# Optimization experiments

Hardware: AMD Instinct MI355X
Metric: run time of the kernel (lower is better)

The kernel has to match this reference:

```python
import jax, jax.numpy as jnp
import numpy as np

N_NODES = 50000
N_EDGES = 600000
D_IN, D_HID, D_OUT = 128, 256, 128


def setup_inputs() -> dict:
    key = jax.random.key(0)
    ks = jax.random.split(key, 8)
    x = jax.random.normal(ks[0], (N_NODES, D_IN), dtype=jnp.float32)
    edge_index = jax.random.randint(ks[1], (2, N_EDGES), 0, N_NODES, dtype=jnp.int64)
    # init_method='uniform' -> edge_weights initialized to ones
    edge_weights = jnp.ones((N_EDGES,), dtype=jnp.float32)
    def lin(k, din, dout):
        s = 1.0 / np.sqrt(din)
        return jax.random.uniform(k, (din, dout), jnp.float32, -s, s)
    W1 = lin(ks[2], D_IN, D_HID)
    b1 = jnp.zeros((D_HID,), jnp.float32)
    W2 = lin(ks[3], D_HID, D_HID)
    b2 = jnp.zeros((D_HID,), jnp.float32)
    W3 = lin(ks[4], D_HID, D_OUT)
    b3 = jnp.zeros((D_OUT,), jnp.float32)
    return {"x": x, "edge_index": edge_index, "edge_weights": edge_weights,
            "W1": W1, "b1": b1, "W2": W2, "b2": b2, "W3": W3, "b3": b3}


def reference(x, edge_index, edge_weights, W1, b1, W2, b2, W3, b3):
    N = x.shape[0]
    # learnable metric: softplus on raw edge weights
    ew = jax.nn.softplus(edge_weights)
    src, dst = edge_index[0], edge_index[1]
    # GCNConv default: add self-loops with weight 1.0
    loop = jnp.arange(N, dtype=edge_index.dtype)
    s = jnp.concatenate([src, loop])
    d = jnp.concatenate([dst, loop])
    w = jnp.concatenate([ew, jnp.ones((N,), ew.dtype)])
    # symmetric degree normalization (gcn_norm); identical edge_weight across layers
    deg = jax.ops.segment_sum(w, d, num_segments=N)
    dinv = jnp.where(deg > 0, jax.lax.rsqrt(deg), jnp.zeros_like(deg))
    norm = dinv[s] * w * dinv[d]  # [E+N]

    def gcn_conv(h, W, b):
        h = h @ W                              # [N, dout]
        msg = h[s] * norm[:, None]             # gather + scale: [E+N, dout]
        out = jax.ops.segment_sum(msg, d, num_segments=N)  # scatter-add
        return out + b

    h = jax.nn.relu(gcn_conv(x, W1, b1))   # dropout p=0.0 -> identity
    h = jax.nn.relu(gcn_conv(h, W2, b2))
    return gcn_conv(h, W3, b3)
```

## Files before the change

### kernel.cpp

```cpp
#include <hip/hip_runtime.h>
#include <hip/hip_fp16.h>
#include <math.h>

#define N_NODES 50000
#define N_EDGES 600000
#define D_IN    128
#define D_HID   256
#define D_OUT   128
#define NB_SCAN ((N_NODES + 255) / 256)

typedef unsigned short u16;
typedef __attribute__((ext_vector_type(8))) _Float16 f16x8;
typedef __attribute__((ext_vector_type(4))) float f32x4;

__device__ __forceinline__ u16 f2h(float x) {
    __half h = __float2half_rn(x);
    return *reinterpret_cast<u16*>(&h);
}
__device__ __forceinline__ float h2f(u16 h) {
    __half hh = *reinterpret_cast<__half*>(&h);
    return __half2float(hh);
}
__device__ __forceinline__ float2 h2f2(unsigned int raw) {
    __half2 h = *reinterpret_cast<__half2*>(&raw);
    return __half22float2(h);
}


__global__ void k_edge_prep(const int* __restrict__ src, const int* __restrict__ dst,
                            const float* __restrict__ w, float* __restrict__ ew,
                            float* __restrict__ deg, int* __restrict__ cnt) {
    int e = blockIdx.x * blockDim.x + threadIdx.x;
    if (e >= N_EDGES) return;
    float x = w[e];
    float sp = fmaxf(x, 0.f) + log1pf(expf(-fabsf(x)));
    ew[e] = sp;
    int d = dst[e];
    atomicAdd(&deg[d], sp);
    atomicAdd(&cnt[d], 1);
    (void)src;
}

__global__ void k_dinv(float* __restrict__ deg) {
    int n = blockIdx.x * blockDim.x + threadIdx.x;
    if (n >= N_NODES) return;
    deg[n] = rsqrtf(deg[n] + 1.0f);
}

__global__ void k_scan1(const int* __restrict__ cnt, int* __restrict__ rowptr,
                        int* __restrict__ bsum) {
    __shared__ int s[256];
    int b = blockIdx.x, t = threadIdx.x;
    int i = b * 256 + t;
    int v = (i < N_NODES) ? cnt[i] : 0;
    s[t] = v;
    __syncthreads();
    for (int off = 1; off < 256; off <<= 1) {
        int u = (t >= off) ? s[t - off] : 0;
        __syncthreads();
        s[t] += u;
        __syncthreads();
    }
    if (i < N_NODES) rowptr[i] = s[t] - v;
    if (t == 255) bsum[b] = s[255];
}

__global__ void k_scan2(const int* __restrict__ bsum, int* __restrict__ boff) {
    __shared__ int s[256];
    int t = threadIdx.x;
    int v = (t < NB_SCAN) ? bsum[t] : 0;
    s[t] = v;
    __syncthreads();
    for (int off = 1; off < 256; off <<= 1) {
        int u = (t >= off) ? s[t - off] : 0;
        __syncthreads();
        s[t] += u;
        __syncthreads();
    }
    if (t < NB_SCAN) boff[t] = s[t] - v;
    if (t == 255) boff[NB_SCAN] = s[255];
}

__global__ void k_scan3(int* __restrict__ rowptr, const int* __restrict__ boff) {
    int b = blockIdx.x, t = threadIdx.x;
    int i = b * 256 + t;
    if (i < N_NODES) rowptr[i] += boff[b];
    if (i == 0) rowptr[N_NODES] = boff[NB_SCAN];
}

__global__ void k_fill(const int* __restrict__ src, const int* __restrict__ dst,
                       const float* __restrict__ ew, const float* __restrict__ dinv,
                       const int* __restrict__ rowptr, int* __restrict__ fill,
                       int2* __restrict__ ecsr) {
    int e = blockIdx.x * blockDim.x + threadIdx.x;
    if (e >= N_EDGES) return;
    int d = dst[e];
    int s = src[e];
    int pos = rowptr[d] + atomicAdd(&fill[d], 1);
    float w = dinv[s] * ew[e] * dinv[d];
    ecsr[pos] = make_int2(s, __float_as_int(w));
}


#define WPREP_TOTAL 131072

__global__ void k_wprep(const float* __restrict__ W1, const float* __restrict__ W2,
                        const float* __restrict__ W3,
                        u16* __restrict__ B1, u16* __restrict__ B2, u16* __restrict__ B3) {
    int idx = blockIdx.x * blockDim.x + threadIdx.x;
    const float* W; u16* B; int K, N, base;
    if (idx < 32768)       { W = W1; B = B1; K = 128; N = 256; base = 0; }
    else if (idx < 98304)  { W = W2; B = B2; K = 256; N = 256; base = 32768; }
    else if (idx < 131072) { W = W3; B = B3; K = 256; N = 128; base = 98304; }
    else return;
    int p = idx - base;
    int n = p % N, k = p / N;
    float x = W[(size_t)k * N + n];
    u16 hi = f2h(x);
    u16 lo = f2h(x - h2f(hi));
    B[(size_t)n * (2 * K) + k] = hi;
    B[(size_t)n * (2 * K) + K + k] = lo;
}


template <int D, int INF, int OUTM, bool BIAS>
__global__ __launch_bounds__(256) void k_agg(const void* __restrict__ inv,
                                             const int* __restrict__ rowptr,
                                             const int2* __restrict__ ecsr,
                                             const float* __restrict__ dinv,
                                             const float* __restrict__ bias,
                                             void* __restrict__ outv) {
    int node = blockIdx.x * 4 + (threadIdx.x >> 6);
    int lane = threadIdx.x & 63;
    if (node >= N_NODES) return;
    float dn = dinv[node];
    float dd = dn * dn;
    int beg = rowptr[node], end = rowptr[node + 1];

    if (D == 256) {
        const float* inf = (const float*)inv;
        const u16* inh = (const u16*)inv;
        float sx, sy, sz, sw;
        if (INF == 0) {
            float4 sv = *(reinterpret_cast<const float4*>(inf + (size_t)node * D) + lane);
            sx = sv.x; sy = sv.y; sz = sv.z; sw = sv.w;
        } else {
            uint2 raw = *reinterpret_cast<const uint2*>(inh + (size_t)node * D + lane * 4);
            float2 f01 = h2f2(raw.x), f23 = h2f2(raw.y);
            sx = f01.x; sy = f01.y; sz = f23.x; sw = f23.y;
        }
        float ax = dd * sx, ay = dd * sy, az = dd * sz, aw = dd * sw;
        int p = beg;
        for (; p + 4 <= end; p += 4) {
            int2 e0 = ecsr[p], e1 = ecsr[p + 1], e2 = ecsr[p + 2], e3 = ecsr[p + 3];
            float w0 = __int_as_float(e0.y), w1 = __int_as_float(e1.y);
            float w2 = __int_as_float(e2.y), w3 = __int_as_float(e3.y);
            if (INF == 0) {
                float4 r0 = *(reinterpret_cast<const float4*>(inf + (size_t)e0.x * D) + lane);
                float4 r1 = *(reinterpret_cast<const float4*>(inf + (size_t)e1.x * D) + lane);
                float4 r2 = *(reinterpret_cast<const float4*>(inf + (size_t)e2.x * D) + lane);
                float4 r3 = *(reinterpret_cast<const float4*>(inf + (size_t)e3.x * D) + lane);
                ax += w0 * r0.x; ay += w0 * r0.y; az += w0 * r0.z; aw += w0 * r0.w;
                ax += w1 * r1.x; ay += w1 * r1.y; az += w1 * r1.z; aw += w1 * r1.w;
                ax += w2 * r2.x; ay += w2 * r2.y; az += w2 * r2.z; aw += w2 * r2.w;
                ax += w3 * r3.x; ay += w3 * r3.y; az += w3 * r3.z; aw += w3 * r3.w;
            } else {
                uint2 q0 = *reinterpret_cast<const uint2*>(inh + (size_t)e0.x * D + lane * 4);
                uint2 q1 = *reinterpret_cast<const uint2*>(inh + (size_t)e1.x * D + lane * 4);
                uint2 q2 = *reinterpret_cast<const uint2*>(inh + (size_t)e2.x * D + lane * 4);
                uint2 q3 = *reinterpret_cast<const uint2*>(inh + (size_t)e3.x * D + lane * 4);
                float2 a0 = h2f2(q0.x), b0 = h2f2(q0.y);
                float2 a1 = h2f2(q1.x), b1 = h2f2(q1.y);
                float2 a2 = h2f2(q2.x), b2 = h2f2(q2.y);
                float2 a3 = h2f2(q3.x), b3 = h2f2(q3.y);
                ax += w0 * a0.x; ay += w0 * a0.y; az += w0 * b0.x; aw += w0 * b0.y;
                ax += w1 * a1.x; ay += w1 * a1.y; az += w1 * b1.x; aw += w1 * b1.y;
                ax += w2 * a2.x; ay += w2 * a2.y; az += w2 * b2.x; aw += w2 * b2.y;
                ax += w3 * a3.x; ay += w3 * a3.y; az += w3 * b3.x; aw += w3 * b3.y;
            }
        }
        for (; p < end; p++) {
            int2 e0 = ecsr[p];
            float w0 = __int_as_float(e0.y);
            if (INF == 0) {
                float4 r0 = *(reinterpret_cast<const float4*>(inf + (size_t)e0.x * D) + lane);
                ax += w0 * r0.x; ay += w0 * r0.y; az += w0 * r0.z; aw += w0 * r0.w;
            } else {
                uint2 q0 = *reinterpret_cast<const uint2*>(inh + (size_t)e0.x * D + lane * 4);
                float2 a0 = h2f2(q0.x), b0 = h2f2(q0.y);
                ax += w0 * a0.x; ay += w0 * a0.y; az += w0 * b0.x; aw += w0 * b0.y;
            }
        }
        if (OUTM == 0) {
            float* out = (float*)outv;
            if (BIAS) {
                float4 b = *(reinterpret_cast<const float4*>(bias) + lane);
                ax += b.x; ay += b.y; az += b.z; aw += b.w;
            }
            float4 res; res.x = ax; res.y = ay; res.z = az; res.w = aw;
            *(reinterpret_cast<float4*>(out + (size_t)node * D) + lane) = res;
        } else {
            u16* out = (u16*)outv;
            ushort4 hv;
            hv.x = f2h(ax); hv.y = f2h(ay); hv.z = f2h(az); hv.w = f2h(aw);
            *reinterpret_cast<ushort4*>(out + (size_t)node * D + lane * 4) = hv;
        }
    } else {
        const float* inf = (const float*)inv;
        const u16* inh = (const u16*)inv;
        float sx, sy;
        if (INF == 0) {
            float2 sv = *(reinterpret_cast<const float2*>(inf + (size_t)node * D) + lane);
            sx = sv.x; sy = sv.y;
        } else {
            unsigned int raw = *reinterpret_cast<const unsigned int*>(inh + (size_t)node * D + lane * 2);
            float2 f = h2f2(raw);
            sx = f.x; sy = f.y;
        }
        float ax = dd * sx, ay = dd * sy;
        int p = beg;
        for (; p + 4 <= end; p += 4) {
            int2 e0 = ecsr[p], e1 = ecsr[p + 1], e2 = ecsr[p + 2], e3 = ecsr[p + 3];
            float w0 = __int_as_float(e0.y), w1 = __int_as_float(e1.y);
            float w2 = __int_as_float(e2.y), w3 = __int_as_float(e3.y);
            if (INF == 0) {
                float2 r0 = *(reinterpret_cast<const float2*>(inf + (size_t)e0.x * D) + lane);
                float2 r1 = *(reinterpret_cast<const float2*>(inf + (size_t)e1.x * D) + lane);
                float2 r2 = *(reinterpret_cast<const float2*>(inf + (size_t)e2.x * D) + lane);
                float2 r3 = *(reinterpret_cast<const float2*>(inf + (size_t)e3.x * D) + lane);
                ax += w0 * r0.x; ay += w0 * r0.y;
                ax += w1 * r1.x; ay += w1 * r1.y;
                ax += w2 * r2.x; ay += w2 * r2.y;
                ax += w3 * r3.x; ay += w3 * r3.y;
            } else {
                unsigned int q0 = *reinterpret_cast<const unsigned int*>(inh + (size_t)e0.x * D + lane * 2);
                unsigned int q1 = *reinterpret_cast<const unsigned int*>(inh + (size_t)e1.x * D + lane * 2);
                unsigned int q2 = *reinterpret_cast<const unsigned int*>(inh + (size_t)e2.x * D + lane * 2);
                unsigned int q3 = *reinterpret_cast<const unsigned int*>(inh + (size_t)e3.x * D + lane * 2);
                float2 f0 = h2f2(q0), f1 = h2f2(q1), f2 = h2f2(q2), f3 = h2f2(q3);
                ax += w0 * f0.x; ay += w0 * f0.y;
                ax += w1 * f1.x; ay += w1 * f1.y;
                ax += w2 * f2.x; ay += w2 * f2.y;
                ax += w3 * f3.x; ay += w3 * f3.y;
            }
        }
        for (; p < end; p++) {
            int2 e0 = ecsr[p];
            float w0 = __int_as_float(e0.y);
            if (INF == 0) {
                float2 r0 = *(reinterpret_cast<const float2*>(inf + (size_t)e0.x * D) + lane);
                ax += w0 * r0.x; ay += w0 * r0.y;
            } else {
                unsigned int q0 = *reinterpret_cast<const unsigned int*>(inh + (size_t)e0.x * D + lane * 2);
                float2 f0 = h2f2(q0);
                ax += w0 * f0.x; ay += w0 * f0.y;
            }
        }
        if (OUTM == 0) {
            float* out = (float*)outv;
            if (BIAS) {
                float2 b = *(reinterpret_cast<const float2*>(bias) + lane);
                ax += b.x; ay += b.y;
            }
            float2 res; res.x = ax; res.y = ay;
            *(reinterpret_cast<float2*>(out + (size_t)node * D) + lane) = res;
        } else {
            u16* out = (u16*)outv;
            ushort2 hv; hv.x = f2h(ax); hv.y = f2h(ay);
            *reinterpret_cast<ushort2*>(out + (size_t)node * D + lane * 2) = hv;
        }
    }
}


template <int OUT, bool BIAS, bool RELU>
__global__ __launch_bounds__(256) void k_gemm_h(const u16* __restrict__ Ap,
                                                const u16* __restrict__ Bp,
                                                const float* __restrict__ bias,
                                                void* __restrict__ Cv,
                                                int M, int K, int NN) {
    const int KP2 = 2 * K;
    __shared__ u16 As[8 * 544];
    __shared__ u16 Bs[2 * 8 * 544];
    int tid = threadIdx.x;
    int bm = blockIdx.y * 128;
    int bn = blockIdx.x * 128;
    int l = tid & 63;
    int w = tid >> 6;
    int wr = w >> 1, wc = w & 1;

    f32x4 zero = {0.f, 0.f, 0.f, 0.f};
    f32x4 acc[4][4];
    #pragma unroll
    for (int i = 0; i < 4; i++)
        #pragma unroll
        for (int j = 0; j < 4; j++) acc[i][j] = zero;

    for (int k0 = 0; k0 < K; k0 += 32) {
        #pragma unroll
        for (int q = 0; q < 2; q++) {
            int idx = tid + q * 256;
            int r = idx >> 2, o = idx & 3;
            int gr = bm + r;
            uint4 va = make_uint4(0u, 0u, 0u, 0u);
            if (gr < M)
                va = *reinterpret_cast<const uint4*>(Ap + (size_t)gr * K + k0 + o * 8);
            *reinterpret_cast<uint4*>(&As[(r >> 4) * 544 + o * 136 + (r & 15) * 8]) = va;
        }
        #pragma unroll
        for (int q = 0; q < 4; q++) {
            int idx = tid + q * 256;
            int r = idx >> 3, oct = idx & 7;
            int hf = oct >> 2, o = oct & 3;
            uint4 vb = *reinterpret_cast<const uint4*>(
                Bp + (size_t)(bn + r) * KP2 + hf * K + k0 + o * 8);
            *reinterpret_cast<uint4*>(
                &Bs[hf * 4352 + (r >> 4) * 544 + o * 136 + (r & 15) * 8]) = vb;
        }
        __syncthreads();
        int fro = (l >> 4) * 136 + (l & 15) * 8;
        f16x8 a[4], bh[4], bl[4];
        #pragma unroll
        for (int i = 0; i < 4; i++)
            a[i] = *reinterpret_cast<const f16x8*>(&As[(wr * 4 + i) * 544 + fro]);
        #pragma unroll
        for (int j = 0; j < 4; j++) {
            bh[j] = *reinterpret_cast<const f16x8*>(&Bs[(wc * 4 + j) * 544 + fro]);
            bl[j] = *reinterpret_cast<const f16x8*>(&Bs[4352 + (wc * 4 + j) * 544 + fro]);
        }
        #pragma unroll
        for (int i = 0; i < 4; i++)
            #pragma unroll
            for (int j = 0; j < 4; j++) {
                acc[i][j] = __builtin_amdgcn_mfma_f32_16x16x32_f16(a[i], bh[j], acc[i][j], 0, 0, 0);
                acc[i][j] = __builtin_amdgcn_mfma_f32_16x16x32_f16(a[i], bl[j], acc[i][j], 0, 0, 0);
            }
        __syncthreads();
    }

    int cl = l & 15;
    int rq = (l >> 4) * 4;
    float bv[4];
    #pragma unroll
    for (int j = 0; j < 4; j++) {
        int gc = bn + wc * 64 + j * 16 + cl;
        bv[j] = BIAS ? bias[gc] : 0.f;
    }
    #pragma unroll
    for (int i = 0; i < 4; i++) {
        #pragma unroll
        for (int r = 0; r < 4; r++) {
            int grow = bm + wr * 64 + i * 16 + rq + r;
            if (grow >= M) continue;
            #pragma unroll
            for (int j = 0; j < 4; j++) {
                int gc = bn + wc * 64 + j * 16 + cl;
                float v = acc[i][j][r];
                if (BIAS) v += bv[j];
                if (RELU) v = fmaxf(v, 0.f);
                if (OUT == 0) {
                    ((float*)Cv)[(size_t)grow * NN + gc] = v;
                } else {
                    ((u16*)Cv)[(size_t)grow * NN + gc] = f2h(v);
                }
            }
        }
    }
}


extern "C" void kernel_launch(void* const* d_in, const int* in_sizes, int n_in,
                              void* d_out, int out_size, void* d_ws, size_t ws_size,
                              hipStream_t stream) {
    const float* x   = (const float*)d_in[0];
    const int*   ei  = (const int*)d_in[1];
    const float* wts = (const float*)d_in[2];
    const float* W1  = (const float*)d_in[3];
    const float* b1  = (const float*)d_in[4];
    const float* W2  = (const float*)d_in[5];
    const float* b2  = (const float*)d_in[6];
    const float* W3  = (const float*)d_in[7];
    const float* b3  = (const float*)d_in[8];
    float* out = (float*)d_out;
    const int* src = ei;
    const int* dst = ei + N_EDGES;

    float* bufA   = (float*)d_ws;
    float* bufB   = bufA + (size_t)N_NODES * D_HID;
    float* ew     = bufB + (size_t)N_NODES * D_HID;
    float* deg    = ew + N_EDGES;
    int*   cnt    = (int*)(deg + N_NODES);
    int*   fill   = cnt + N_NODES;
    int*   rowptr = fill + N_NODES;
    int2*  ecsr   = (int2*)(rowptr + (N_NODES + 2));
    u16*   Wb1    = (u16*)(ecsr + N_EDGES);
    u16*   Wb2    = Wb1 + 256 * 256;
    u16*   Wb3    = Wb2 + 256 * 512;
    int*   bsum   = (int*)(Wb3 + 128 * 512);
    int*   boff   = bsum + NB_SCAN;

    hipMemsetAsync(deg, 0, sizeof(float) * N_NODES + sizeof(int) * 2 * N_NODES, stream);

    int ethreads = 256;
    int eblocks = (N_EDGES + ethreads - 1) / ethreads;
    k_edge_prep<<<eblocks, ethreads, 0, stream>>>(src, dst, wts, ew, deg, cnt);
    k_dinv<<<(N_NODES + 255) / 256, 256, 0, stream>>>(deg);
    k_scan1<<<NB_SCAN, 256, 0, stream>>>(cnt, rowptr, bsum);
    k_scan2<<<1, 256, 0, stream>>>(bsum, boff);
    k_scan3<<<NB_SCAN, 256, 0, stream>>>(rowptr, boff);
    k_fill<<<eblocks, ethreads, 0, stream>>>(src, dst, ew, deg, rowptr, fill, ecsr);
    k_wprep<<<(WPREP_TOTAL + 255) / 256, 256, 0, stream>>>(W1, W2, W3, Wb1, Wb2, Wb3);

    int aggBlocks = (N_NODES + 3) / 4;
    int gy = (N_NODES + 127) / 128;

    k_agg<128, 0, 1, false><<<aggBlocks, 256, 0, stream>>>(x, rowptr, ecsr, deg, nullptr, bufA);
    {
        dim3 g(2, gy);
        k_gemm_h<1, true, true><<<g, 256, 0, stream>>>((const u16*)bufA, Wb1, b1, bufB,
                                                       N_NODES, D_IN, D_HID);
    }
    k_agg<256, 1, 1, false><<<aggBlocks, 256, 0, stream>>>(bufB, rowptr, ecsr, deg, nullptr, bufA);
    {
        dim3 g(2, gy);
        k_gemm_h<1, true, true><<<g, 256, 0, stream>>>((const u16*)bufA, Wb2, b2, bufB,
                                                       N_NODES, D_HID, D_HID);
    }
    {
        dim3 g(1, gy);
        k_gemm_h<1, false, false><<<g, 256, 0, stream>>>((const u16*)bufB, Wb3, nullptr, bufA,
                                                         N_NODES, D_HID, D_OUT);
    }
    k_agg<128, 1, 0, true><<<aggBlocks, 256, 0, stream>>>(bufA, rowptr, ecsr, deg, b3, out);
}
```

Baseline: 384.2 us.

## Replace float degree atomics with CSR-based degree sum and atomic-free fill

Edge preprocessing now records each edge's rank from the count atomic, which lets the CSR fill run without a second atomic pass. The float atomicAdd degree accumulation is dropped. The degree is instead summed per node from the CSR rows, and normalization becomes a separate per-node pass over the CSR. This removes a set of float atomics and the fill atomics, but adds two thread-per-node kernels with serial, uncoalesced row loops and an extra rank array.

```diff
diff --git a/kernel.cpp b/kernel.cpp
--- a/kernel.cpp
+++ b/kernel.cpp
@@ -27,24 +27,14 @@
 }
 
 
-__global__ void k_edge_prep(const int* __restrict__ src, const int* __restrict__ dst,
-                            const float* __restrict__ w, float* __restrict__ ew,
-                            float* __restrict__ deg, int* __restrict__ cnt) {
+__global__ void k_hist(const int* __restrict__ dst, const float* __restrict__ w,
+                       float* __restrict__ ew, int* __restrict__ rank,
+                       int* __restrict__ cnt) {
     int e = blockIdx.x * blockDim.x + threadIdx.x;
     if (e >= N_EDGES) return;
     float x = w[e];
-    float sp = fmaxf(x, 0.f) + log1pf(expf(-fabsf(x)));
-    ew[e] = sp;
-    int d = dst[e];
-    atomicAdd(&deg[d], sp);
-    atomicAdd(&cnt[d], 1);
-    (void)src;
-}
-
-__global__ void k_dinv(float* __restrict__ deg) {
-    int n = blockIdx.x * blockDim.x + threadIdx.x;
-    if (n >= N_NODES) return;
-    deg[n] = rsqrtf(deg[n] + 1.0f);
+    ew[e] = fmaxf(x, 0.f) + log1pf(expf(-fabsf(x)));
+    rank[e] = atomicAdd(&cnt[dst[e]], 1);
 }
 
 __global__ void k_scan1(const int* __restrict__ cnt, int* __restrict__ rowptr,
@@ -88,17 +78,36 @@
     if (i == 0) rowptr[N_NODES] = boff[NB_SCAN];
 }
 
-__global__ void k_fill(const int* __restrict__ src, const int* __restrict__ dst,
-                       const float* __restrict__ ew, const float* __restrict__ dinv,
-                       const int* __restrict__ rowptr, int* __restrict__ fill,
-                       int2* __restrict__ ecsr) {
+__global__ void k_fill2(const int* __restrict__ src, const int* __restrict__ dst,
+                        const float* __restrict__ ew, const int* __restrict__ rank,
+                        const int* __restrict__ rowptr, int2* __restrict__ ecsr) {
     int e = blockIdx.x * blockDim.x + threadIdx.x;
     if (e >= N_EDGES) return;
-    int d = dst[e];
-    int s = src[e];
-    int pos = rowptr[d] + atomicAdd(&fill[d], 1);
-    float w = dinv[s] * ew[e] * dinv[d];
-    ecsr[pos] = make_int2(s, __float_as_int(w));
+    int pos = rowptr[dst[e]] + rank[e];
+    ecsr[pos] = make_int2(src[e], __float_as_int(ew[e]));
+}
+
+__global__ void k_degdinv(const int* __restrict__ rowptr, const int2* __restrict__ ecsr,
+                          float* __restrict__ dinv) {
+    int n = blockIdx.x * blockDim.x + threadIdx.x;
+    if (n >= N_NODES) return;
+    int beg = rowptr[n], end = rowptr[n + 1];
+    float s = 1.0f;
+    for (int p = beg; p < end; p++) s += __int_as_float(ecsr[p].y);
+    dinv[n] = rsqrtf(s);
+}
+
+__global__ void k_norm(const int* __restrict__ rowptr, const float* __restrict__ dinv,
+                       int2* __restrict__ ecsr) {
+    int n = blockIdx.x * blockDim.x + threadIdx.x;
+    if (n >= N_NODES) return;
+    int beg = rowptr[n], end = rowptr[n + 1];
+    float dn = dinv[n];
+    for (int p = beg; p < end; p++) {
+        int2 r = ecsr[p];
+        float w = dinv[r.x] * __int_as_float(r.y) * dn;
+        ecsr[p] = make_int2(r.x, __float_as_int(w));
+    }
 }
 
 
@@ -388,10 +397,10 @@
     float* bufA   = (float*)d_ws;
     float* bufB   = bufA + (size_t)N_NODES * D_HID;
     float* ew     = bufB + (size_t)N_NODES * D_HID;
-    float* deg    = ew + N_EDGES;
-    int*   cnt    = (int*)(deg + N_NODES);
-    int*   fill   = cnt + N_NODES;
-    int*   rowptr = fill + N_NODES;
+    float* dinv   = ew + N_EDGES;
+    int*   cnt    = (int*)(dinv + N_NODES);
+    int*   rank   = cnt + N_NODES;
+    int*   rowptr = rank + N_EDGES;
     int2*  ecsr   = (int2*)(rowptr + (N_NODES + 2));
     u16*   Wb1    = (u16*)(ecsr + N_EDGES);
     u16*   Wb2    = Wb1 + 256 * 256;
@@ -399,28 +408,30 @@
     int*   bsum   = (int*)(Wb3 + 128 * 512);
     int*   boff   = bsum + NB_SCAN;
 
-    hipMemsetAsync(deg, 0, sizeof(float) * N_NODES + sizeof(int) * 2 * N_NODES, stream);
+    hipMemsetAsync(cnt, 0, sizeof(int) * N_NODES, stream);
 
     int ethreads = 256;
     int eblocks = (N_EDGES + ethreads - 1) / ethreads;
-    k_edge_prep<<<eblocks, ethreads, 0, stream>>>(src, dst, wts, ew, deg, cnt);
-    k_dinv<<<(N_NODES + 255) / 256, 256, 0, stream>>>(deg);
+    int nblocks = (N_NODES + 255) / 256;
+    k_hist<<<eblocks, ethreads, 0, stream>>>(dst, wts, ew, rank, cnt);
     k_scan1<<<NB_SCAN, 256, 0, stream>>>(cnt, rowptr, bsum);
     k_scan2<<<1, 256, 0, stream>>>(bsum, boff);
     k_scan3<<<NB_SCAN, 256, 0, stream>>>(rowptr, boff);
-    k_fill<<<eblocks, ethreads, 0, stream>>>(src, dst, ew, deg, rowptr, fill, ecsr);
+    k_fill2<<<eblocks, ethreads, 0, stream>>>(src, dst, ew, rank, rowptr, ecsr);
+    k_degdinv<<<nblocks, 256, 0, stream>>>(rowptr, ecsr, dinv);
+    k_norm<<<nblocks, 256, 0, stream>>>(rowptr, dinv, ecsr);
     k_wprep<<<(WPREP_TOTAL + 255) / 256, 256, 0, stream>>>(W1, W2, W3, Wb1, Wb2, Wb3);
 
     int aggBlocks = (N_NODES + 3) / 4;
     int gy = (N_NODES + 127) / 128;
 
-    k_agg<128, 0, 1, false><<<aggBlocks, 256, 0, stream>>>(x, rowptr, ecsr, deg, nullptr, bufA);
+    k_agg<128, 0, 1, false><<<aggBlocks, 256, 0, stream>>>(x, rowptr, ecsr, dinv, nullptr, bufA);
     {
         dim3 g(2, gy);
         k_gemm_h<1, true, true><<<g, 256, 0, stream>>>((const u16*)bufA, Wb1, b1, bufB,
                                                        N_NODES, D_IN, D_HID);
     }
-    k_agg<256, 1, 1, false><<<aggBlocks, 256, 0, stream>>>(bufB, rowptr, ecsr, deg, nullptr, bufA);
+    k_agg<256, 1, 1, false><<<aggBlocks, 256, 0, stream>>>(bufB, rowptr, ecsr, dinv, nullptr, bufA);
     {
         dim3 g(2, gy);
         k_gemm_h<1, true, true><<<g, 256, 0, stream>>>((const u16*)bufA, Wb2, b2, bufB,
@@ -431,5 +442,5 @@
         k_gemm_h<1, false, false><<<g, 256, 0, stream>>>((const u16*)bufB, Wb3, nullptr, bufA,
                                                          N_NODES, D_HID, D_OUT);
     }
-    k_agg<128, 1, 0, true><<<aggBlocks, 256, 0, stream>>>(bufA, rowptr, ecsr, deg, b3, out);
-}
+    k_agg<128, 1, 0, true><<<aggBlocks, 256, 0, stream>>>(bufA, rowptr, ecsr, dinv, b3, out);
+}
```

After: 346.7 us. 9.8% less time.
